# Optimization experiments

Measured on AMD Instinct MI355X. Metric: run time of the kernel, lower is better.

The kernel has to match this reference:

```python
import jax, jax.numpy as jnp
import numpy as np

N_VERT = 163842  # icosphere level-7 vertex count
IN_FEATS = 64
OUT_FEATS = 64
BATCH = 2
K = 7  # center vertex + 6 one-ring neighbors


def setup_inputs() -> dict:
    key = jax.random.key(0)
    k1, k2, k3, k4 = jax.random.split(key, 4)
    x = jax.random.normal(k1, (N_VERT, IN_FEATS, BATCH), dtype=jnp.float32)
    neigh_orders = jax.random.randint(k2, (K * N_VERT,), 0, N_VERT, dtype=jnp.int64)
    W = jax.random.normal(k3, (OUT_FEATS, K * IN_FEATS), dtype=jnp.float32) * 0.05
    b = jax.random.normal(k4, (OUT_FEATS,), dtype=jnp.float32) * 0.05
    return {"x": x, "neigh_orders": neigh_orders, "W": W, "b": b}


def reference(x, neigh_orders, W, b):
    # x: [N, C, B]; neigh_orders: [7N] flat indices, grouped per-vertex (n*7 + k)
    N = x.shape[0]
    C = x.shape[1]
    idx = neigh_orders.reshape(N, K)            # [N, 7]
    gathered = x[idx]                           # [N, 7, C, B] irregular gather
    Wr = W.reshape(W.shape[0], K, C)            # [O, 7, C] matches flatten order (k*C + c)
    # out[n, o, b] = sum_{k,c} gathered[n,k,c,b] * W[o, k*C + c] + b[o]
    out = jnp.einsum("nkcb,okc->nob", gathered, Wr) + b[None, :, None]
    return out  # [N, O, B]
```

## Files before the change

kernel.cpp:

```cpp
#include <hip/hip_runtime.h>

#define NV      163842
#define CIN     64
#define KN      7
#define NKMAX   (NV * KN)
#define KDIM    448
#define KSTEPS  14
#define VPC     16
#define ROWS    32
#define ASTRIDE 456

typedef short  short8 __attribute__((ext_vector_type(8)));
typedef float  f32x4  __attribute__((ext_vector_type(4)));

static __device__ __forceinline__ unsigned int pack_bf16(float a, float b) {
#if __has_builtin(__builtin_amdgcn_cvt_pk_bf16_f32)
    typedef __bf16 bf16x2 __attribute__((ext_vector_type(2)));
    union { bf16x2 v; unsigned int u; } cv;
    cv.v = __builtin_amdgcn_cvt_pk_bf16_f32(a, b);
    return cv.u;
#else
    unsigned int ua = __float_as_uint(a);
    unsigned int ub = __float_as_uint(b);
    ua = (ua + 0x7FFFu + ((ua >> 16) & 1u)) >> 16;
    ub = (ub + 0x7FFFu + ((ub >> 16) & 1u)) & 0xFFFF0000u;
    return ua | ub;
#endif
}

static __device__ __forceinline__ void bar_lgkm() {
    asm volatile("s_waitcnt lgkmcnt(0)\n\ts_barrier" ::: "memory");
}

__global__ __launch_bounds__(256)
void xcast(const float* __restrict__ x, unsigned int* __restrict__ xt, int nf4)
{
    const int f = blockIdx.x * 256 + threadIdx.x;
    if (f >= nf4) return;
    const f32x4 g = __builtin_nontemporal_load(&((const f32x4*)x)[f]);
    const int v = f >> 5;
    const int r = f & 31;
    xt[v * 32 + r]           = pack_bf16(g[0], g[2]);
    xt[NV * 32 + v * 32 + r] = pack_bf16(g[1], g[3]);
}

__global__ __launch_bounds__(256, 3)
void onering_mfma_bf16(const unsigned short* __restrict__ xt,
                       const int* __restrict__ neigh,
                       const float* __restrict__ W,
                       const float* __restrict__ bias,
                       float* __restrict__ out,
                       int nchunks)
{
    __shared__ unsigned short A_lds[ROWS * ASTRIDE];
    __shared__ float          C_lds[VPC * 128];

    const int tid  = threadIdx.x;
    const int lane = tid & 63;
    const int w    = tid >> 6;
    const int ncol = lane & 15;
    const int kgrp = lane >> 4;
    const int G    = gridDim.x;

    short8 bfrag[KSTEPS];
    {
        const int o = w * 16 + ncol;
#pragma unroll
        for (int s = 0; s < KSTEPS; ++s) {
            const int kb = s * 32 + kgrp * 8;
            const float4* wp = (const float4*)(W + o * KDIM + kb);
            float4 w0 = wp[0];
            float4 w1 = wp[1];
            union { short8 v; unsigned int u[4]; } pk;
            pk.u[0] = pack_bf16(w0.x, w0.y);
            pk.u[1] = pack_bf16(w0.z, w0.w);
            pk.u[2] = pack_bf16(w1.x, w1.y);
            pk.u[3] = pack_bf16(w1.z, w1.w);
            bfrag[s] = pk.v;
        }
    }
    const float biasv = bias[w * 16 + ncol];

    const int l8 = tid & 7;
    int nidx[7];
    int lbyte[7];
    int soff[7];
#pragma unroll
    for (int i = 0; i < 7; ++i) {
        const int seg = (tid >> 3) + 32 * i;
        const int row = seg / 7;
        const int k   = seg - row * 7;
        const int lv  = row >> 1, bb = row & 1;
        nidx[i]  = lv * KN + k;
        lbyte[i] = row * (ASTRIDE * 2) + k * 128 + l8 * 16;
        soff[i]  = bb * (NV * 64) + l8 * 8;
    }

    const int ch0 = blockIdx.x;
    int    I[7];
    short8 R[7];

#pragma unroll
    for (int i = 0; i < 7; ++i) {
        int gi = ch0 * (VPC * KN) + nidx[i];
        I[i] = __builtin_nontemporal_load(&neigh[gi < NKMAX ? gi : 0]);
    }
#pragma unroll
    for (int i = 0; i < 7; ++i)
        R[i] = *(const short8*)(xt + soff[i] + I[i] * 64);
#pragma unroll
    for (int i = 0; i < 7; ++i) {
        int gi = (ch0 + G) * (VPC * KN) + nidx[i];
        I[i] = __builtin_nontemporal_load(&neigh[gi < NKMAX ? gi : 0]);
    }

    for (int ch = ch0; ch < nchunks; ch += G) {
        const int vb = ch * VPC;

        bar_lgkm();

#pragma unroll
        for (int i = 0; i < 7; ++i)
            *(short8*)((char*)A_lds + lbyte[i]) = R[i];
#pragma unroll
        for (int i = 0; i < 7; ++i)
            R[i] = *(const short8*)(xt + soff[i] + I[i] * 64);
#pragma unroll
        for (int i = 0; i < 7; ++i) {
            int gi = (ch + 2 * G) * (VPC * KN) + nidx[i];
            I[i] = __builtin_nontemporal_load(&neigh[gi < NKMAX ? gi : 0]);
        }

        bar_lgkm();

        f32x4 acc0 = {0.f, 0.f, 0.f, 0.f};
        f32x4 acc1 = {0.f, 0.f, 0.f, 0.f};
#pragma unroll
        for (int s = 0; s < KSTEPS; ++s) {
            const int kb = s * 32 + kgrp * 8;
            const short8 a0 = *(const short8*)&A_lds[ncol * ASTRIDE + kb];
            const short8 a1 = *(const short8*)&A_lds[(16 + ncol) * ASTRIDE + kb];
            acc0 = __builtin_amdgcn_mfma_f32_16x16x32_bf16(a0, bfrag[s], acc0, 0, 0, 0);
            acc1 = __builtin_amdgcn_mfma_f32_16x16x32_bf16(a1, bfrag[s], acc1, 0, 0, 0);
        }

        const int o2 = (w * 16 + ncol) * 2;
#pragma unroll
        for (int j = 0; j < 4; ++j) {
            const int r  = kgrp * 4 + j;
            C_lds[(r >> 1) * 128 + o2 + (r & 1)] = acc0[j] + biasv;
            const int r2 = 16 + r;
            C_lds[(r2 >> 1) * 128 + o2 + (r2 & 1)] = acc1[j] + biasv;
        }

        bar_lgkm();

        f32x4* dst = (f32x4*)(out + vb * 128);
#pragma unroll
        for (int it = 0; it < 2; ++it) {
            const int fidx = tid + 256 * it;
            if (vb + (fidx >> 5) < NV)
                __builtin_nontemporal_store(((const f32x4*)C_lds)[fidx], &dst[fidx]);
        }
    }
}

__global__ __launch_bounds__(256, 4)
void onering_mfma_f32(const float* __restrict__ x,
                      const int* __restrict__ neigh,
                      const float* __restrict__ W,
                      const float* __restrict__ bias,
                      float* __restrict__ out,
                      int nchunks)
{
    __shared__ unsigned short A_lds[ROWS * ASTRIDE];
    const int tid  = threadIdx.x;
    const int lane = tid & 63;
    const int w    = tid >> 6;
    const int ncol = lane & 15;
    const int kgrp = lane >> 4;

    short8 bfrag[KSTEPS];
    {
        const int o = w * 16 + ncol;
#pragma unroll
        for (int s = 0; s < KSTEPS; ++s) {
            const int kb = s * 32 + kgrp * 8;
            const float4* wp = (const float4*)(W + o * KDIM + kb);
            float4 w0 = wp[0];
            float4 w1 = wp[1];
            union { short8 v; unsigned int u[4]; } pk;
            pk.u[0] = pack_bf16(w0.x, w0.y);
            pk.u[1] = pack_bf16(w0.z, w0.w);
            pk.u[2] = pack_bf16(w1.x, w1.y);
            pk.u[3] = pack_bf16(w1.z, w1.w);
            bfrag[s] = pk.v;
        }
    }
    const float biasv = bias[w * 16 + ncol];
    const int off4  = tid & 31;
    const int sbase = tid >> 5;

    for (int ch = blockIdx.x; ch < nchunks; ch += gridDim.x) {
        const int vb = ch * VPC;
        __syncthreads();
#pragma unroll
        for (int i = 0; i < 14; ++i) {
            const int s  = sbase + 8 * i;
            const int lv = s / 7;
            const int k  = s - lv * 7;
            const int n  = vb + lv;
            int vi = 0;
            if (n < NV) vi = neigh[n * KN + k];
            const float4 g = ((const float4*)x)[vi * 32 + off4];
            const int base = k * 64 + 2 * off4;
            ((unsigned int*)A_lds)[((lv * 2)     * ASTRIDE + base) >> 1] = pack_bf16(g.x, g.z);
            ((unsigned int*)A_lds)[((lv * 2 + 1) * ASTRIDE + base) >> 1] = pack_bf16(g.y, g.w);
        }
        __syncthreads();
        f32x4 acc0 = {0.f, 0.f, 0.f, 0.f};
        f32x4 acc1 = {0.f, 0.f, 0.f, 0.f};
#pragma unroll
        for (int s = 0; s < KSTEPS; ++s) {
            const int kb = s * 32 + kgrp * 8;
            const short8 a0 = *(const short8*)&A_lds[ncol * ASTRIDE + kb];
            const short8 a1 = *(const short8*)&A_lds[(16 + ncol) * ASTRIDE + kb];
            acc0 = __builtin_amdgcn_mfma_f32_16x16x32_bf16(a0, bfrag[s], acc0, 0, 0, 0);
            acc1 = __builtin_amdgcn_mfma_f32_16x16x32_bf16(a1, bfrag[s], acc1, 0, 0, 0);
        }
        const int o = w * 16 + ncol;
#pragma unroll
        for (int j = 0; j < 4; ++j) {
            const int r = kgrp * 4 + j;
            {
                const int lv = r >> 1, bb = r & 1, n = vb + lv;
                if (n < NV) out[n * 128 + o * 2 + bb] = acc0[j] + biasv;
            }
            {
                const int m = 16 + r;
                const int lv = m >> 1, bb = m & 1, n = vb + lv;
                if (n < NV) out[n * 128 + o * 2 + bb] = acc1[j] + biasv;
            }
        }
    }
}

extern "C" void kernel_launch(void* const* d_in, const int* in_sizes, int n_in,
                              void* d_out, int out_size, void* d_ws, size_t ws_size,
                              hipStream_t stream) {
    const float* x     = (const float*)d_in[0];
    const int*   neigh = (const int*)d_in[1];
    const float* W     = (const float*)d_in[2];
    const float* bias  = (const float*)d_in[3];
    float*       out   = (float*)d_out;

    const int nchunks = (NV + VPC - 1) / VPC;
    const size_t need = (size_t)2 * NV * 64 * sizeof(unsigned short);

    if (ws_size >= need) {
        unsigned short* xt = (unsigned short*)d_ws;
        const int nf4 = NV * 32;
        xcast<<<dim3((nf4 + 255) / 256), dim3(256), 0, stream>>>(x, (unsigned int*)xt, nf4);
        onering_mfma_bf16<<<dim3(2560), dim3(256), 0, stream>>>(xt, neigh, W, bias, out, nchunks);
    } else {
        onering_mfma_f32<<<dim3(2560), dim3(256), 0, stream>>>(x, neigh, W, bias, out, nchunks);
    }
}
```

Before: 212.3 us.

## Double-buffer gather LDS, widen blocks to 512 threads, store MFMA results directly

The bf16 one-ring kernel now uses 512-thread blocks whose 8 waves split the 32 gathered rows into two halves. Each wave runs a single 16x16 MFMA accumulator instead of two. The gathered A tile is double-buffered in LDS and the prefetch depth grows by one chunk, so each iteration needs one barrier instead of two. Results go straight from registers to global memory as 8-byte nontemporal stores, dropping the C_lds staging buffer. In exchange the global writes are narrower and less coalesced, and the grid shrinks to 1024 blocks.

```diff
diff --git a/kernel.cpp b/kernel.cpp
--- a/kernel.cpp
+++ b/kernel.cpp
@@ -9,9 +9,11 @@
 #define VPC     16
 #define ROWS    32
 #define ASTRIDE 456
+#define ABUF    (ROWS * ASTRIDE)
 
 typedef short  short8 __attribute__((ext_vector_type(8)));
 typedef float  f32x4  __attribute__((ext_vector_type(4)));
+typedef float  f32x2  __attribute__((ext_vector_type(2)));
 
 static __device__ __forceinline__ unsigned int pack_bf16(float a, float b) {
 #if __has_builtin(__builtin_amdgcn_cvt_pk_bf16_f32)
@@ -44,27 +46,28 @@
     xt[NV * 32 + v * 32 + r] = pack_bf16(g[1], g[3]);
 }
 
-__global__ __launch_bounds__(256, 3)
-void onering_mfma_bf16(const unsigned short* __restrict__ xt,
-                       const int* __restrict__ neigh,
-                       const float* __restrict__ W,
-                       const float* __restrict__ bias,
-                       float* __restrict__ out,
-                       int nchunks)
+__global__ __launch_bounds__(512, 4)
+void onering_mfma_bf16_v2(const unsigned short* __restrict__ xt,
+                          const int* __restrict__ neigh,
+                          const float* __restrict__ W,
+                          const float* __restrict__ bias,
+                          float* __restrict__ out,
+                          int nchunks)
 {
-    __shared__ unsigned short A_lds[ROWS * ASTRIDE];
-    __shared__ float          C_lds[VPC * 128];
+    __shared__ __align__(16) unsigned short A_lds[2 * ABUF];
 
     const int tid  = threadIdx.x;
     const int lane = tid & 63;
-    const int w    = tid >> 6;
+    const int wid  = tid >> 6;
+    const int wc   = wid & 3;
+    const int wr   = wid >> 2;
     const int ncol = lane & 15;
     const int kgrp = lane >> 4;
     const int G    = gridDim.x;
 
     short8 bfrag[KSTEPS];
     {
-        const int o = w * 16 + ncol;
+        const int o = wc * 16 + ncol;
 #pragma unroll
         for (int s = 0; s < KSTEPS; ++s) {
             const int kb = s * 32 + kgrp * 8;
@@ -79,15 +82,15 @@
             bfrag[s] = pk.v;
         }
     }
-    const float biasv = bias[w * 16 + ncol];
+    const float biasv = bias[wc * 16 + ncol];
 
     const int l8 = tid & 7;
-    int nidx[7];
-    int lbyte[7];
-    int soff[7];
-#pragma unroll
-    for (int i = 0; i < 7; ++i) {
-        const int seg = (tid >> 3) + 32 * i;
+    int nidx[4];
+    int lbyte[4];
+    int soff[4];
+#pragma unroll
+    for (int i = 0; i < 4; ++i) {
+        const int seg = (tid >> 3) + 64 * i;
         const int row = seg / 7;
         const int k   = seg - row * 7;
         const int lv  = row >> 1, bb = row & 1;
@@ -95,73 +98,80 @@
         lbyte[i] = row * (ASTRIDE * 2) + k * 128 + l8 * 16;
         soff[i]  = bb * (NV * 64) + l8 * 8;
     }
+    const bool act3 = (tid < 256);
 
     const int ch0 = blockIdx.x;
-    int    I[7];
-    short8 R[7];
-
-#pragma unroll
-    for (int i = 0; i < 7; ++i) {
-        int gi = ch0 * (VPC * KN) + nidx[i];
-        I[i] = __builtin_nontemporal_load(&neigh[gi < NKMAX ? gi : 0]);
-    }
-#pragma unroll
-    for (int i = 0; i < 7; ++i)
-        R[i] = *(const short8*)(xt + soff[i] + I[i] * 64);
-#pragma unroll
-    for (int i = 0; i < 7; ++i) {
-        int gi = (ch0 + G) * (VPC * KN) + nidx[i];
-        I[i] = __builtin_nontemporal_load(&neigh[gi < NKMAX ? gi : 0]);
-    }
-
+    int    I[4];
+    short8 R[4];
+
+#pragma unroll
+    for (int i = 0; i < 4; ++i)
+        if (i < 3 || act3) {
+            int gi = ch0 * (VPC * KN) + nidx[i];
+            I[i] = __builtin_nontemporal_load(&neigh[gi < NKMAX ? gi : 0]);
+        }
+#pragma unroll
+    for (int i = 0; i < 4; ++i)
+        if (i < 3 || act3) R[i] = *(const short8*)(xt + soff[i] + I[i] * 64);
+#pragma unroll
+    for (int i = 0; i < 4; ++i)
+        if (i < 3 || act3) *(short8*)((char*)A_lds + lbyte[i]) = R[i];
+#pragma unroll
+    for (int i = 0; i < 4; ++i)
+        if (i < 3 || act3) {
+            int gi = (ch0 + G) * (VPC * KN) + nidx[i];
+            I[i] = __builtin_nontemporal_load(&neigh[gi < NKMAX ? gi : 0]);
+        }
+#pragma unroll
+    for (int i = 0; i < 4; ++i)
+        if (i < 3 || act3) R[i] = *(const short8*)(xt + soff[i] + I[i] * 64);
+#pragma unroll
+    for (int i = 0; i < 4; ++i)
+        if (i < 3 || act3) {
+            int gi = (ch0 + 2 * G) * (VPC * KN) + nidx[i];
+            I[i] = __builtin_nontemporal_load(&neigh[gi < NKMAX ? gi : 0]);
+        }
+    bar_lgkm();
+
+    int rbuf = 0;
     for (int ch = ch0; ch < nchunks; ch += G) {
         const int vb = ch * VPC;
 
+        char* wbase = (char*)A_lds + (rbuf ^ 1) * (ABUF * 2);
+#pragma unroll
+        for (int i = 0; i < 4; ++i)
+            if (i < 3 || act3) *(short8*)(wbase + lbyte[i]) = R[i];
+#pragma unroll
+        for (int i = 0; i < 4; ++i)
+            if (i < 3 || act3) R[i] = *(const short8*)(xt + soff[i] + I[i] * 64);
+#pragma unroll
+        for (int i = 0; i < 4; ++i)
+            if (i < 3 || act3) {
+                int gi = (ch + 3 * G) * (VPC * KN) + nidx[i];
+                I[i] = __builtin_nontemporal_load(&neigh[gi < NKMAX ? gi : 0]);
+            }
+
+        const unsigned short* Ap = A_lds + rbuf * ABUF + (wr * 16 + ncol) * ASTRIDE;
+        f32x4 acc = {0.f, 0.f, 0.f, 0.f};
+#pragma unroll
+        for (int s = 0; s < KSTEPS; ++s) {
+            const short8 a = *(const short8*)&Ap[s * 32 + kgrp * 8];
+            acc = __builtin_amdgcn_mfma_f32_16x16x32_bf16(a, bfrag[s], acc, 0, 0, 0);
+        }
+
+        const int ocol = (wc * 16 + ncol) * 2;
+        const int v0   = vb + wr * 8 + kgrp * 2;
+#pragma unroll
+        for (int jp = 0; jp < 2; ++jp) {
+            const int n = v0 + jp;
+            if (n < NV) {
+                f32x2 val = { acc[2 * jp] + biasv, acc[2 * jp + 1] + biasv };
+                __builtin_nontemporal_store(val, (f32x2*)(out + (size_t)n * 128 + ocol));
+            }
+        }
+
         bar_lgkm();
-
-#pragma unroll
-        for (int i = 0; i < 7; ++i)
-            *(short8*)((char*)A_lds + lbyte[i]) = R[i];
-#pragma unroll
-        for (int i = 0; i < 7; ++i)
-            R[i] = *(const short8*)(xt + soff[i] + I[i] * 64);
-#pragma unroll
-        for (int i = 0; i < 7; ++i) {
-            int gi = (ch + 2 * G) * (VPC * KN) + nidx[i];
-            I[i] = __builtin_nontemporal_load(&neigh[gi < NKMAX ? gi : 0]);
-        }
-
-        bar_lgkm();
-
-        f32x4 acc0 = {0.f, 0.f, 0.f, 0.f};
-        f32x4 acc1 = {0.f, 0.f, 0.f, 0.f};
-#pragma unroll
-        for (int s = 0; s < KSTEPS; ++s) {
-            const int kb = s * 32 + kgrp * 8;
-            const short8 a0 = *(const short8*)&A_lds[ncol * ASTRIDE + kb];
-            const short8 a1 = *(const short8*)&A_lds[(16 + ncol) * ASTRIDE + kb];
-            acc0 = __builtin_amdgcn_mfma_f32_16x16x32_bf16(a0, bfrag[s], acc0, 0, 0, 0);
-            acc1 = __builtin_amdgcn_mfma_f32_16x16x32_bf16(a1, bfrag[s], acc1, 0, 0, 0);
-        }
-
-        const int o2 = (w * 16 + ncol) * 2;
-#pragma unroll
-        for (int j = 0; j < 4; ++j) {
-            const int r  = kgrp * 4 + j;
-            C_lds[(r >> 1) * 128 + o2 + (r & 1)] = acc0[j] + biasv;
-            const int r2 = 16 + r;
-            C_lds[(r2 >> 1) * 128 + o2 + (r2 & 1)] = acc1[j] + biasv;
-        }
-
-        bar_lgkm();
-
-        f32x4* dst = (f32x4*)(out + vb * 128);
-#pragma unroll
-        for (int it = 0; it < 2; ++it) {
-            const int fidx = tid + 256 * it;
-            if (vb + (fidx >> 5) < NV)
-                __builtin_nontemporal_store(((const f32x4*)C_lds)[fidx], &dst[fidx]);
-        }
+        rbuf ^= 1;
     }
 }
 
@@ -261,7 +271,7 @@
         unsigned short* xt = (unsigned short*)d_ws;
         const int nf4 = NV * 32;
         xcast<<<dim3((nf4 + 255) / 256), dim3(256), 0, stream>>>(x, (unsigned int*)xt, nf4);
-        onering_mfma_bf16<<<dim3(2560), dim3(256), 0, stream>>>(xt, neigh, W, bias, out, nchunks);
+        onering_mfma_bf16_v2<<<dim3(1024), dim3(512), 0, stream>>>(xt, neigh, W, bias, out, nchunks);
     } else {
         onering_mfma_f32<<<dim3(2560), dim3(256), 0, stream>>>(x, neigh, W, bias, out, nchunks);
     }
```

Measured after the change: 248.3 us. 1.17x slower.

## Double-buffer LDS A tile, deepen prefetch, and retile waves to 2x2 layout

Applied to the files above, without the earlier changes.

Stages the gathered A tile in two LDS buffers so the MFMA loop on one buffer overlaps the LDS writes and global gathers for the next chunk, leaving one barrier per chunk instead of three. Prefetch depth increases to three chunks ahead. Waves are remapped to a 2x2 layout where each wave computes 16 rows by 32 outputs, reusing one A fragment for two MFMAs. Each wave now writes its own output through a private C slice. The cost is more registers (two B fragment arrays), more LDS, occupancy cut from 3 to 2 blocks, and a smaller grid of 2048.

```diff
diff --git a/kernel.cpp b/kernel.cpp
--- a/kernel.cpp
+++ b/kernel.cpp
@@ -9,9 +9,11 @@
 #define VPC     16
 #define ROWS    32
 #define ASTRIDE 456
+#define ABUF    (ROWS * ASTRIDE)
 
 typedef short  short8 __attribute__((ext_vector_type(8)));
 typedef float  f32x4  __attribute__((ext_vector_type(4)));
+typedef float  f32x2  __attribute__((ext_vector_type(2)));
 
 static __device__ __forceinline__ unsigned int pack_bf16(float a, float b) {
 #if __has_builtin(__builtin_amdgcn_cvt_pk_bf16_f32)
@@ -44,42 +46,52 @@
     xt[NV * 32 + v * 32 + r] = pack_bf16(g[1], g[3]);
 }
 
-__global__ __launch_bounds__(256, 3)
-void onering_mfma_bf16(const unsigned short* __restrict__ xt,
-                       const int* __restrict__ neigh,
-                       const float* __restrict__ W,
-                       const float* __restrict__ bias,
-                       float* __restrict__ out,
-                       int nchunks)
+__global__ __launch_bounds__(256, 2)
+void onering_mfma_bf16_v3(const unsigned short* __restrict__ xt,
+                          const int* __restrict__ neigh,
+                          const float* __restrict__ W,
+                          const float* __restrict__ bias,
+                          float* __restrict__ out,
+                          int nchunks)
 {
-    __shared__ unsigned short A_lds[ROWS * ASTRIDE];
-    __shared__ float          C_lds[VPC * 128];
+    __shared__ __align__(16) unsigned short A_lds[2 * ABUF];
+    __shared__ __align__(16) float          C_lds[4 * 512];
 
     const int tid  = threadIdx.x;
     const int lane = tid & 63;
     const int w    = tid >> 6;
+    const int wc   = w & 1;
+    const int wr   = w >> 1;
     const int ncol = lane & 15;
     const int kgrp = lane >> 4;
     const int G    = gridDim.x;
 
-    short8 bfrag[KSTEPS];
+    short8 bfrag0[KSTEPS], bfrag1[KSTEPS];
+    const int o0 = wc * 32 + ncol;
+    const int o1 = o0 + 16;
     {
-        const int o = w * 16 + ncol;
 #pragma unroll
         for (int s = 0; s < KSTEPS; ++s) {
             const int kb = s * 32 + kgrp * 8;
-            const float4* wp = (const float4*)(W + o * KDIM + kb);
-            float4 w0 = wp[0];
-            float4 w1 = wp[1];
+            const float4* wp0 = (const float4*)(W + o0 * KDIM + kb);
+            const float4* wp1 = (const float4*)(W + o1 * KDIM + kb);
+            float4 a0 = wp0[0], a1 = wp0[1];
+            float4 b0 = wp1[0], b1 = wp1[1];
             union { short8 v; unsigned int u[4]; } pk;
-            pk.u[0] = pack_bf16(w0.x, w0.y);
-            pk.u[1] = pack_bf16(w0.z, w0.w);
-            pk.u[2] = pack_bf16(w1.x, w1.y);
-            pk.u[3] = pack_bf16(w1.z, w1.w);
-            bfrag[s] = pk.v;
-        }
-    }
-    const float biasv = bias[w * 16 + ncol];
+            pk.u[0] = pack_bf16(a0.x, a0.y);
+            pk.u[1] = pack_bf16(a0.z, a0.w);
+            pk.u[2] = pack_bf16(a1.x, a1.y);
+            pk.u[3] = pack_bf16(a1.z, a1.w);
+            bfrag0[s] = pk.v;
+            pk.u[0] = pack_bf16(b0.x, b0.y);
+            pk.u[1] = pack_bf16(b0.z, b0.w);
+            pk.u[2] = pack_bf16(b1.x, b1.y);
+            pk.u[3] = pack_bf16(b1.z, b1.w);
+            bfrag1[s] = pk.v;
+        }
+    }
+    const float bias0 = bias[o0];
+    const float bias1 = bias[o1];
 
     const int l8 = tid & 7;
     int nidx[7];
@@ -109,59 +121,76 @@
     for (int i = 0; i < 7; ++i)
         R[i] = *(const short8*)(xt + soff[i] + I[i] * 64);
 #pragma unroll
+    for (int i = 0; i < 7; ++i)
+        *(short8*)((char*)A_lds + lbyte[i]) = R[i];
+#pragma unroll
     for (int i = 0; i < 7; ++i) {
         int gi = (ch0 + G) * (VPC * KN) + nidx[i];
         I[i] = __builtin_nontemporal_load(&neigh[gi < NKMAX ? gi : 0]);
     }
+#pragma unroll
+    for (int i = 0; i < 7; ++i)
+        R[i] = *(const short8*)(xt + soff[i] + I[i] * 64);
+#pragma unroll
+    for (int i = 0; i < 7; ++i) {
+        int gi = (ch0 + 2 * G) * (VPC * KN) + nidx[i];
+        I[i] = __builtin_nontemporal_load(&neigh[gi < NKMAX ? gi : 0]);
+    }
+    bar_lgkm();
+
+    int rbuf = 0;
+    float* const Cw = C_lds + w * 512;
+    const int vt0 = wr * 8;
+    const int cb  = wc * 64;
 
     for (int ch = ch0; ch < nchunks; ch += G) {
         const int vb = ch * VPC;
 
-        bar_lgkm();
-
+        const unsigned short* Ap = A_lds + rbuf * ABUF + (wr * 16 + ncol) * ASTRIDE;
+        f32x4 acc0 = {0.f, 0.f, 0.f, 0.f};
+        f32x4 acc1 = {0.f, 0.f, 0.f, 0.f};
+#pragma unroll
+        for (int s = 0; s < KSTEPS; ++s) {
+            const short8 a = *(const short8*)&Ap[s * 32 + kgrp * 8];
+            acc0 = __builtin_amdgcn_mfma_f32_16x16x32_bf16(a, bfrag0[s], acc0, 0, 0, 0);
+            acc1 = __builtin_amdgcn_mfma_f32_16x16x32_bf16(a, bfrag1[s], acc1, 0, 0, 0);
+        }
+
+        char* wbase = (char*)A_lds + (rbuf ^ 1) * (ABUF * 2);
 #pragma unroll
         for (int i = 0; i < 7; ++i)
-            *(short8*)((char*)A_lds + lbyte[i]) = R[i];
+            *(short8*)(wbase + lbyte[i]) = R[i];
 #pragma unroll
         for (int i = 0; i < 7; ++i)
             R[i] = *(const short8*)(xt + soff[i] + I[i] * 64);
 #pragma unroll
         for (int i = 0; i < 7; ++i) {
-            int gi = (ch + 2 * G) * (VPC * KN) + nidx[i];
+            int gi = (ch + 3 * G) * (VPC * KN) + nidx[i];
             I[i] = __builtin_nontemporal_load(&neigh[gi < NKMAX ? gi : 0]);
         }
 
+#pragma unroll
+        for (int p = 0; p < 2; ++p) {
+            const int lvv = kgrp * 2 + p;
+            f32x2 v0 = { acc0[2 * p] + bias0, acc0[2 * p + 1] + bias0 };
+            f32x2 v1 = { acc1[2 * p] + bias1, acc1[2 * p + 1] + bias1 };
+            *(f32x2*)&Cw[lvv * 64 + ncol * 2]        = v0;
+            *(f32x2*)&Cw[lvv * 64 + (16 + ncol) * 2] = v1;
+        }
+#pragma unroll
+        for (int i = 0; i < 2; ++i) {
+            const int fo  = (i * 64 + lane) * 4;
+            const int lvv = fo >> 6;
+            const int rem = fo & 63;
+            const int n   = vb + vt0 + lvv;
+            if (n < NV) {
+                f32x4 val = *(const f32x4*)&Cw[fo];
+                __builtin_nontemporal_store(val, (f32x4*)(out + (size_t)n * 128 + cb + rem));
+            }
+        }
+
         bar_lgkm();
-
-        f32x4 acc0 = {0.f, 0.f, 0.f, 0.f};
-        f32x4 acc1 = {0.f, 0.f, 0.f, 0.f};
-#pragma unroll
-        for (int s = 0; s < KSTEPS; ++s) {
-            const int kb = s * 32 + kgrp * 8;
-            const short8 a0 = *(const short8*)&A_lds[ncol * ASTRIDE + kb];
-            const short8 a1 = *(const short8*)&A_lds[(16 + ncol) * ASTRIDE + kb];
-            acc0 = __builtin_amdgcn_mfma_f32_16x16x32_bf16(a0, bfrag[s], acc0, 0, 0, 0);
-            acc1 = __builtin_amdgcn_mfma_f32_16x16x32_bf16(a1, bfrag[s], acc1, 0, 0, 0);
-        }
-
-        const int o2 = (w * 16 + ncol) * 2;
-#pragma unroll
-        for (int j = 0; j < 4; ++j) {
-            const int r  = kgrp * 4 + j;
-            C_lds[(r >> 1) * 128 + o2 + (r & 1)] = acc0[j] + biasv;
-            const int r2 = 16 + r;
-            C_lds[(r2 >> 1) * 128 + o2 + (r2 & 1)] = acc1[j] + biasv;
-        }
-
-        bar_lgkm();
-
-        f32x4* dst = (f32x4*)(out + vb * 128);
-#pragma unroll
-        for (int it = 0; it < 2; ++it) {
-            const int fidx = tid + 256 * it;
-            if (vb + (fidx >> 5) < NV)
-                __builtin_nontemporal_store(((const f32x4*)C_lds)[fidx], &dst[fidx]);
-        }
+        rbuf ^= 1;
     }
 }
 
@@ -261,7 +290,7 @@
         unsigned short* xt = (unsigned short*)d_ws;
         const int nf4 = NV * 32;
         xcast<<<dim3((nf4 + 255) / 256), dim3(256), 0, stream>>>(x, (unsigned int*)xt, nf4);
-        onering_mfma_bf16<<<dim3(2560), dim3(256), 0, stream>>>(xt, neigh, W, bias, out, nchunks);
+        onering_mfma_bf16_v3<<<dim3(2048), dim3(256), 0, stream>>>(xt, neigh, W, bias, out, nchunks);
     } else {
         onering_mfma_f32<<<dim3(2560), dim3(256), 0, stream>>>(x, neigh, W, bias, out, nchunks);
     }
```

Result: slower. 257.7 us (+21.4%).
